# Kernel optimization log

Hardware: AMD Instinct MI355X
Metric: run time of the kernel (lower is better)

The kernel has to match this reference:

```python
import jax, jax.numpy as jnp
import numpy as np

# Standard NF4 quantization codebook (bitsandbytes values)
_NF4_CB = np.array([
    -1.0, -0.6961928009986877, -0.5250730514526367, -0.39491748809814453,
    -0.28444138169288635, -0.18477343022823334, -0.09105003625154495, 0.0,
    0.07958029955625534, 0.16093020141124725, 0.24611230194568634, 0.33791524171829224,
    0.44070982933044434, 0.5626170039176941, 0.7229568362236023, 1.0], dtype=np.float32)

B, L, H, E, DFF = 2, 2048, 2048, 8, 8192
BLK = 512  # NF4 quantization block size (b_idx = h // 512 in kernel)


def setup_inputs() -> dict:
    key = jax.random.key(0)
    ks = jax.random.split(key, 8)
    N = B * L
    x = jax.random.normal(ks[0], (B, L, H), dtype=jnp.float32)
    router_w = jax.random.normal(ks[1], (H, E), dtype=jnp.float32) * 0.02
    # packed NF4: one byte = two 4-bit codebook indices (low nibble -> even h)
    nf4 = jax.random.randint(ks[2], (N, E, H // 2), 0, 256, dtype=jnp.int32)
    mean = jax.random.normal(ks[3], (N, E, H // BLK), dtype=jnp.float32) * 0.01
    std = jax.random.uniform(ks[4], (N, E, H // BLK), dtype=jnp.float32) + 0.5
    codebook = jnp.asarray(_NF4_CB)
    w1 = jax.random.normal(ks[5], (H, DFF), dtype=jnp.float32) * 0.02
    w2 = jax.random.normal(ks[6], (DFF, H), dtype=jnp.float32) * 0.02
    return {"x": x, "router_w": router_w, "nf4": nf4, "mean": mean,
            "std": std, "codebook": codebook, "w1": w1, "w2": w2}


def reference(x, router_w, nf4, mean, std, codebook, w1, w2):
    b, l, h = x.shape
    n = b * l
    e = router_w.shape[1]
    xf = x.reshape(n, h)

    # shared expert MLP (base_mlp): Linear -> GELU -> Linear
    mlp = jax.nn.gelu(xf @ w1) @ w2  # [N, H]

    # router: logits in fp32, softmax, cast to fp16 as the kernel does
    logits = xf @ router_w  # [N, E]
    probs = jax.nn.softmax(logits, axis=-1).astype(jnp.float16).astype(jnp.float32)

    # NF4 unpack: low nibble -> even h, high nibble -> odd h
    low = nf4 & 15
    high = (nf4 >> 4) & 15
    idx = jnp.stack([low, high], axis=-1).reshape(n, e, h)  # interleave -> [N,E,H]
    vals = codebook[idx]  # codebook gather, [N,E,H]

    # per-block (512) rescale: val*std + mean
    nb = mean.shape[-1]
    blk = h // nb
    dq = (vals.reshape(n, e, nb, blk) * std[..., None] + mean[..., None]).reshape(n, e, h)

    # weighted expert mix + MLP residual add
    moe = jnp.einsum('ne,neh->nh', probs, dq)
    return (moe + mlp).reshape(b, l, h)
```

## Files before the change

kernel.cpp:

```cpp
#include <hip/hip_runtime.h>
#include <hip/hip_bf16.h>
#include <hip/hip_fp16.h>

#define H 2048
#define E 8
#define DFF 8192
#define NTOK 4096
#define NB 4

typedef _Float16 f16x8 __attribute__((ext_vector_type(8)));
typedef _Float16 f16x2 __attribute__((ext_vector_type(2)));
typedef float f32x4 __attribute__((ext_vector_type(4)));

#define AS1 __attribute__((address_space(1)))
#define AS3 __attribute__((address_space(3)))

__device__ __forceinline__ void gl_lds16(const void* g, void* l) {
    __builtin_amdgcn_global_load_lds((const AS1 unsigned int*)g,
                                     (AS3 unsigned int*)l, 16, 0, 0);
}

__device__ __forceinline__ float gelu_f(float x) {
    float u = 0.7978845608028654f * x * (1.0f + 0.044715f * x * x);
    float t = fabsf(u);
    float e = __expf(-2.0f * t);
    float th = (1.0f - e) / (1.0f + e);
    th = copysignf(th, u);
    return 0.5f * x * (1.0f + th);
}

__global__ __launch_bounds__(256) void router_moe_kernel(
    const float* __restrict__ x, const float* __restrict__ rw,
    const int* __restrict__ nf4, const float* __restrict__ mean,
    const float* __restrict__ stdv, const float* __restrict__ cb,
    _Float16* __restrict__ xh, float* __restrict__ moe)
{
    int n = blockIdx.x, t = threadIdx.x;
    __shared__ float red[4][E];
    __shared__ float pr[E];
    __shared__ float cbl[32];
    __shared__ float ps[E][NB];
    __shared__ float cmean[NB];

    float acc[E];
#pragma unroll
    for (int e = 0; e < E; ++e) acc[e] = 0.f;
    const float* xr = x + (size_t)n * H;
#pragma unroll
    for (int k = 0; k < H / 256; ++k) {
        int h = t + k * 256;
        float xv = xr[h];
        xh[(size_t)n * H + h] = (_Float16)xv;
        const float4* r4 = reinterpret_cast<const float4*>(rw + (size_t)h * E);
        float4 a = r4[0], b = r4[1];
        acc[0] += xv * a.x; acc[1] += xv * a.y; acc[2] += xv * a.z; acc[3] += xv * a.w;
        acc[4] += xv * b.x; acc[5] += xv * b.y; acc[6] += xv * b.z; acc[7] += xv * b.w;
    }
#pragma unroll
    for (int e = 0; e < E; ++e) {
        float v = acc[e];
#pragma unroll
        for (int o = 32; o > 0; o >>= 1) v += __shfl_down(v, o, 64);
        acc[e] = v;
    }
    int wave = t >> 6, lane = t & 63;
    if (lane == 0) {
#pragma unroll
        for (int e = 0; e < E; ++e) red[wave][e] = acc[e];
    }
    __syncthreads();
    if (t == 0) {
        float lg[E];
        float mx = -1e30f;
#pragma unroll
        for (int e = 0; e < E; ++e) {
            lg[e] = red[0][e] + red[1][e] + red[2][e] + red[3][e];
            mx = fmaxf(mx, lg[e]);
        }
        float s = 0.f;
#pragma unroll
        for (int e = 0; e < E; ++e) { lg[e] = expf(lg[e] - mx); s += lg[e]; }
        float inv = 1.f / s;
#pragma unroll
        for (int e = 0; e < E; ++e) {
            float p = lg[e] * inv;
            pr[e] = __half2float(__float2half(p));
        }
    }
    __syncthreads();

    if (t < 16) { float v = cb[t]; cbl[t] = v; cbl[t + 16] = v; }
    else if (t >= 32 && t < 64) {
        int e = (t - 32) >> 2, b = t & 3;
        ps[e][b] = pr[e] * stdv[((size_t)n * E + e) * NB + b];
    } else if (t >= 64 && t < 68) {
        int b = t - 64; float s = 0.f;
        for (int e = 0; e < E; ++e)
            s += pr[e] * mean[((size_t)n * E + e) * NB + b];
        cmean[b] = s;
    }
    __syncthreads();

    int b = t >> 6;
    int cboff = (t & 1) << 4;
    const int4* w4 = reinterpret_cast<const int4*>(nf4 + (size_t)n * (E * H / 2));
    float o[8];
    float cm = cmean[b];
#pragma unroll
    for (int u = 0; u < 8; ++u) o[u] = cm;
#pragma unroll
    for (int e = 0; e < E; ++e) {
        int4 wv = w4[e * 256 + t];
        float pse = ps[e][b];
        int w0 = wv.x, w1 = wv.y, w2 = wv.z, w3 = wv.w;
        o[0] += pse * cbl[(w0 & 15) + cboff];
        o[1] += pse * cbl[((w0 >> 4) & 15) + cboff];
        o[2] += pse * cbl[(w1 & 15) + cboff];
        o[3] += pse * cbl[((w1 >> 4) & 15) + cboff];
        o[4] += pse * cbl[(w2 & 15) + cboff];
        o[5] += pse * cbl[((w2 >> 4) & 15) + cboff];
        o[6] += pse * cbl[(w3 & 15) + cboff];
        o[7] += pse * cbl[((w3 >> 4) & 15) + cboff];
    }
    float4* op = reinterpret_cast<float4*>(moe + (size_t)n * H + 8 * t);
    op[0] = make_float4(o[0], o[1], o[2], o[3]);
    op[1] = make_float4(o[4], o[5], o[6], o[7]);
}

__global__ __launch_bounds__(256) void transpose_cast_kernel(
    const float* __restrict__ src, _Float16* __restrict__ dst, int R, int C)
{
    __shared__ float tile[64][65];
    int t = threadIdx.x;
    int c0 = blockIdx.x * 64, r0 = blockIdx.y * 64;
    int ct = (t & 15) * 4, rt = t >> 4;
#pragma unroll
    for (int i = 0; i < 4; ++i) {
        int r = rt + i * 16;
        float4 v = *reinterpret_cast<const float4*>(src + (size_t)(r0 + r) * C + c0 + ct);
        tile[r][ct] = v.x; tile[r][ct + 1] = v.y;
        tile[r][ct + 2] = v.z; tile[r][ct + 3] = v.w;
    }
    __syncthreads();
    int u = (t & 31) * 2, cq = t >> 5;
#pragma unroll
    for (int i = 0; i < 8; ++i) {
        int c = cq + i * 8;
        f16x2 pk;
        pk[0] = (_Float16)tile[u][c];
        pk[1] = (_Float16)tile[u + 1][c];
        *reinterpret_cast<f16x2*>(dst + (size_t)(c0 + c) * R + r0 + u) = pk;
    }
}

template <int EPI, int MAP>
__global__ __launch_bounds__(512, 2) void gemm8p_kernel(
    const _Float16* __restrict__ A, const _Float16* __restrict__ Bt,
    const float* __restrict__ addsrc, void* __restrict__ outv,
    float* __restrict__ aux, int K, int LDK, int N)
{
    __shared__ uint4 lds_u4[131072 / 16];
    char* lds = (char*)lds_u4;
    char* R0 = lds;
    char* R1 = lds + 65536;

    int t = threadIdx.x;
    int id = blockIdx.x;
    int xcd = id & 7, chunk = id >> 3;
    int by, bx, ks = 0;
    if constexpr (MAP == 0) {
        by = (xcd & 1) * 8 + (chunk & 7);
        bx = (xcd >> 1) * 8 + (chunk >> 3);
    } else {
        by = (xcd >> 1) * 4 + (chunk & 3);
        bx = (xcd & 1) * 4 + ((chunk >> 2) & 3);
        ks = chunk >> 4;
    }
    int m0 = by * 256, n0 = bx * 256;
    int koff = ks * K;

    const unsigned short* sA = (const unsigned short*)A
        + (size_t)(m0 + (t & 255)) * LDK + koff + (t >> 8) * 8;
    const unsigned short* sB = (const unsigned short*)Bt
        + (size_t)(n0 + (t & 255)) * LDK + koff + (t >> 8) * 8;
    unsigned dstT = (unsigned)t * 16;

    int lane = t & 63, wave = t >> 6;
    int wr = wave >> 2, wc = wave & 3;
    int mb = wr * 128, nb = wc * 64;
    int q = lane >> 4, m16 = lane & 15;

    unsigned aBase = (unsigned)(mb + m16) * 16u;
    unsigned bBase = 32768u + (unsigned)(nb + m16) * 16u;

    f32x4 acc[8][4] = {};
    f16x8 af[8], bL[4], bH[4];

#define STG_A(Wb, T, s) do { \
    gl_lds16(sA + (size_t)(T) * 64 + (s) * 16,      (Wb) + (s) * 8192 + dstT); \
    gl_lds16(sA + (size_t)(T) * 64 + (s) * 16 + 16, (Wb) + (s) * 8192 + 8192 + dstT); } while (0)
#define STG_B(Wb, T, s) do { \
    gl_lds16(sB + (size_t)(T) * 64 + (s) * 16,      (Wb) + 32768 + (s) * 8192 + dstT); \
    gl_lds16(sB + (size_t)(T) * 64 + (s) * 16 + 16, (Wb) + 32768 + (s) * 8192 + 8192 + dstT); } while (0)
#define RD_A(Rb, ih) do { \
    _Pragma("unroll") for (int il = 0; il < 4; ++il) \
    _Pragma("unroll") for (int kh = 0; kh < 2; ++kh) \
        af[il * 2 + kh] = *(const f16x8*)((Rb) + aBase + \
            (unsigned)(kh * 16384 + q * 4096 + (ih) * 1024 + il * 256)); } while (0)
#define RD_B(Rb, jh, dst) do { \
    _Pragma("unroll") for (int jl = 0; jl < 2; ++jl) \
    _Pragma("unroll") for (int kh = 0; kh < 2; ++kh) \
        dst[jl * 2 + kh] = *(const f16x8*)((Rb) + bBase + \
            (unsigned)(kh * 16384 + q * 4096 + (jh) * 512 + jl * 256)); } while (0)
#define MMQ(ih, bfr, j0) do { \
    __builtin_amdgcn_s_setprio(1); \
    _Pragma("unroll") for (int il = 0; il < 4; ++il) \
    _Pragma("unroll") for (int jl = 0; jl < 2; ++jl) \
    _Pragma("unroll") for (int kh = 0; kh < 2; ++kh) \
        acc[(ih) * 4 + il][(j0) + jl] = __builtin_amdgcn_mfma_f32_16x16x32_f16( \
            af[il * 2 + kh], bfr[jl * 2 + kh], acc[(ih) * 4 + il][(j0) + jl], 0, 0, 0); \
    __builtin_amdgcn_s_setprio(0); } while (0)
#define BARR  asm volatile("s_barrier" ::: "memory")
#define LGKM0 asm volatile("s_waitcnt lgkmcnt(0)" ::: "memory")

    STG_A(R0, 0, 0); STG_A(R0, 0, 2);
    STG_B(R0, 0, 0); STG_B(R0, 0, 2);
    STG_A(R1, 1, 0);
    asm volatile("s_waitcnt vmcnt(2)" ::: "memory");
    BARR;

    int NIT = K / 128;
    for (int i = 0; i < NIT; ++i) {
        int T0 = 2 * i, T1 = 2 * i + 1;
        bool more = (i + 1 < NIT);

        STG_A(R1, T1, 2);
        RD_A(R0, 0); RD_B(R0, 0, bL);
        BARR; LGKM0;
        MMQ(0, bL, 0);
        BARR;
        STG_B(R1, T1, 0);
        RD_B(R0, 1, bH);
        BARR; LGKM0;
        MMQ(0, bH, 2);
        BARR;
        STG_B(R1, T1, 2);
        RD_A(R0, 1);
        BARR; LGKM0;
        MMQ(1, bH, 2);
        BARR;
        if (more) STG_A(R0, T0 + 2, 0);
        MMQ(1, bL, 0);
        if (more) asm volatile("s_waitcnt vmcnt(2)" ::: "memory");
        else      asm volatile("s_waitcnt vmcnt(0)" ::: "memory");
        BARR;

        if (more) STG_A(R0, T0 + 2, 2);
        RD_A(R1, 0); RD_B(R1, 0, bL);
        BARR; LGKM0;
        MMQ(0, bL, 0);
        BARR;
        if (more) STG_B(R0, T0 + 2, 0);
        RD_B(R1, 1, bH);
        BARR; LGKM0;
        MMQ(0, bH, 2);
        BARR;
        if (more) STG_B(R0, T0 + 2, 2);
        RD_A(R1, 1);
        BARR; LGKM0;
        MMQ(1, bH, 2);
        BARR;
        if (more) STG_A(R1, T1 + 2, 0);
        MMQ(1, bL, 0);
        if (more) asm volatile("s_waitcnt vmcnt(2)" ::: "memory");
        else      asm volatile("s_waitcnt vmcnt(0)" ::: "memory");
        BARR;
    }

#pragma unroll
    for (int i = 0; i < 8; ++i)
#pragma unroll
        for (int j = 0; j < 4; ++j) {
            int row = m0 + mb + i * 16 + q * 4;
            int col = n0 + nb + j * 16 + m16;
#pragma unroll
            for (int rix = 0; rix < 4; ++rix) {
                float v = acc[i][j][rix];
                size_t o = (size_t)(row + rix) * N + col;
                if constexpr (EPI == 0) {
                    ((_Float16*)outv)[o] = (_Float16)gelu_f(v);
                } else {
                    if (ks == 0) ((float*)outv)[o] = v + addsrc[o];
                    else         aux[o] = v;
                }
            }
        }
#undef STG_A
#undef STG_B
#undef RD_A
#undef RD_B
#undef MMQ
#undef BARR
#undef LGKM0
}

__global__ __launch_bounds__(256) void combine_kernel(
    float* __restrict__ out, const float* __restrict__ part)
{
    size_t base = (size_t)blockIdx.x * 256 + threadIdx.x;
    const float4* p4 = (const float4*)part;
    float4* o4 = (float4*)out;
#pragma unroll
    for (int s = 0; s < 4; ++s) {
        size_t i = base + (size_t)s * 524288;
        float4 a = o4[i], b = p4[i];
        o4[i] = make_float4(a.x + b.x, a.y + b.y, a.z + b.z, a.w + b.w);
    }
}

extern "C" void kernel_launch(void* const* d_in, const int* in_sizes, int n_in,
                              void* d_out, int out_size, void* d_ws, size_t ws_size,
                              hipStream_t stream) {
    const float* x    = (const float*)d_in[0];
    const float* rw   = (const float*)d_in[1];
    const int*   nf4  = (const int*)d_in[2];
    const float* mean = (const float*)d_in[3];
    const float* stdv = (const float*)d_in[4];
    const float* cb   = (const float*)d_in[5];
    const float* w1   = (const float*)d_in[6];
    const float* w2   = (const float*)d_in[7];
    float* out = (float*)d_out;

    char* ws = (char*)d_ws;
    float* moe        = (float*)(ws + 131072);
    _Float16* xh      = (_Float16*)(ws + 33685504);
    _Float16* w1t     = (_Float16*)(ws + 50462720);
    _Float16* w2t     = (_Float16*)(ws + 84017152);
    _Float16* hid     = (_Float16*)(ws + 117571584);
    float* pbuf       = (float*)(ws + 50462720);

    router_moe_kernel<<<NTOK, 256, 0, stream>>>(x, rw, nf4, mean, stdv, cb, xh, moe);
    transpose_cast_kernel<<<dim3(DFF / 64, H / 64), 256, 0, stream>>>(w1, w1t, H, DFF);
    transpose_cast_kernel<<<dim3(H / 64, DFF / 64), 256, 0, stream>>>(w2, w2t, DFF, H);
    gemm8p_kernel<0, 0><<<512, 512, 0, stream>>>(xh, w1t, nullptr, (void*)hid,
                                                 nullptr, H, H, DFF);
    gemm8p_kernel<1, 1><<<256, 512, 0, stream>>>(hid, w2t, moe, (void*)out,
                                                 pbuf, DFF / 2, DFF, H);
    combine_kernel<<<2048, 256, 0, stream>>>(out, pbuf);
}
```

Before: 737.0 us.

## Replace double-buffered K=128 GEMM pipeline with five-stage K=32 ring buffer

```diff
diff --git a/kernel.cpp b/kernel.cpp
--- a/kernel.cpp
+++ b/kernel.cpp
@@ -154,15 +154,13 @@
 }
 
 template <int EPI, int MAP>
-__global__ __launch_bounds__(512, 2) void gemm8p_kernel(
+__global__ __launch_bounds__(512, 2) void gemm5b_kernel(
     const _Float16* __restrict__ A, const _Float16* __restrict__ Bt,
     const float* __restrict__ addsrc, void* __restrict__ outv,
     float* __restrict__ aux, int K, int LDK, int N)
 {
-    __shared__ uint4 lds_u4[131072 / 16];
+    __shared__ uint4 lds_u4[163840 / 16];
     char* lds = (char*)lds_u4;
-    char* R0 = lds;
-    char* R1 = lds + 65536;
 
     int t = threadIdx.x;
     int id = blockIdx.x;
@@ -190,91 +188,65 @@
     int mb = wr * 128, nb = wc * 64;
     int q = lane >> 4, m16 = lane & 15;
 
-    unsigned aBase = (unsigned)(mb + m16) * 16u;
-    unsigned bBase = 32768u + (unsigned)(nb + m16) * 16u;
+    unsigned aOff = (unsigned)(q * 4096 + (mb + m16) * 16);
+    unsigned bOff = (unsigned)(16384 + q * 4096 + (nb + m16) * 16);
 
     f32x4 acc[8][4] = {};
-    f16x8 af[8], bL[4], bH[4];
-
-#define STG_A(Wb, T, s) do { \
-    gl_lds16(sA + (size_t)(T) * 64 + (s) * 16,      (Wb) + (s) * 8192 + dstT); \
-    gl_lds16(sA + (size_t)(T) * 64 + (s) * 16 + 16, (Wb) + (s) * 8192 + 8192 + dstT); } while (0)
-#define STG_B(Wb, T, s) do { \
-    gl_lds16(sB + (size_t)(T) * 64 + (s) * 16,      (Wb) + 32768 + (s) * 8192 + dstT); \
-    gl_lds16(sB + (size_t)(T) * 64 + (s) * 16 + 16, (Wb) + 32768 + (s) * 8192 + 8192 + dstT); } while (0)
-#define RD_A(Rb, ih) do { \
+    f16x8 afL[4], afH[4], bf[4];
+
+#define STG_A(Wb, T) do { \
+    gl_lds16(sA + (size_t)(T) * 32,      (Wb) + dstT); \
+    gl_lds16(sA + (size_t)(T) * 32 + 16, (Wb) + 8192 + dstT); } while (0)
+#define STG_B(Wb, T) do { \
+    gl_lds16(sB + (size_t)(T) * 32,      (Wb) + 16384 + dstT); \
+    gl_lds16(sB + (size_t)(T) * 32 + 16, (Wb) + 16384 + 8192 + dstT); } while (0)
+#define RD_B(Rb) do { \
+    _Pragma("unroll") for (int jl = 0; jl < 4; ++jl) \
+        bf[jl] = *(const f16x8*)((Rb) + bOff + jl * 256); } while (0)
+#define RD_AL(Rb) do { \
     _Pragma("unroll") for (int il = 0; il < 4; ++il) \
-    _Pragma("unroll") for (int kh = 0; kh < 2; ++kh) \
-        af[il * 2 + kh] = *(const f16x8*)((Rb) + aBase + \
-            (unsigned)(kh * 16384 + q * 4096 + (ih) * 1024 + il * 256)); } while (0)
-#define RD_B(Rb, jh, dst) do { \
-    _Pragma("unroll") for (int jl = 0; jl < 2; ++jl) \
-    _Pragma("unroll") for (int kh = 0; kh < 2; ++kh) \
-        dst[jl * 2 + kh] = *(const f16x8*)((Rb) + bBase + \
-            (unsigned)(kh * 16384 + q * 4096 + (jh) * 512 + jl * 256)); } while (0)
-#define MMQ(ih, bfr, j0) do { \
+        afL[il] = *(const f16x8*)((Rb) + aOff + il * 256); } while (0)
+#define RD_AH(Rb) do { \
+    _Pragma("unroll") for (int il = 0; il < 4; ++il) \
+        afH[il] = *(const f16x8*)((Rb) + aOff + 1024 + il * 256); } while (0)
+#define MM(i0, afr) do { \
     __builtin_amdgcn_s_setprio(1); \
     _Pragma("unroll") for (int il = 0; il < 4; ++il) \
-    _Pragma("unroll") for (int jl = 0; jl < 2; ++jl) \
-    _Pragma("unroll") for (int kh = 0; kh < 2; ++kh) \
-        acc[(ih) * 4 + il][(j0) + jl] = __builtin_amdgcn_mfma_f32_16x16x32_f16( \
-            af[il * 2 + kh], bfr[jl * 2 + kh], acc[(ih) * 4 + il][(j0) + jl], 0, 0, 0); \
+    _Pragma("unroll") for (int jl = 0; jl < 4; ++jl) \
+        acc[(i0) + il][jl] = __builtin_amdgcn_mfma_f32_16x16x32_f16( \
+            afr[il], bf[jl], acc[(i0) + il][jl], 0, 0, 0); \
     __builtin_amdgcn_s_setprio(0); } while (0)
 #define BARR  asm volatile("s_barrier" ::: "memory")
 #define LGKM0 asm volatile("s_waitcnt lgkmcnt(0)" ::: "memory")
 
-    STG_A(R0, 0, 0); STG_A(R0, 0, 2);
-    STG_B(R0, 0, 0); STG_B(R0, 0, 2);
-    STG_A(R1, 1, 0);
-    asm volatile("s_waitcnt vmcnt(2)" ::: "memory");
+    STG_A(lds,         0); STG_B(lds,         0);
+    STG_A(lds + 32768, 1); STG_B(lds + 32768, 1);
+    STG_A(lds + 65536, 2); STG_B(lds + 65536, 2);
+    asm volatile("s_waitcnt vmcnt(8)" ::: "memory");
     BARR;
 
-    int NIT = K / 128;
-    for (int i = 0; i < NIT; ++i) {
-        int T0 = 2 * i, T1 = 2 * i + 1;
-        bool more = (i + 1 < NIT);
-
-        STG_A(R1, T1, 2);
-        RD_A(R0, 0); RD_B(R0, 0, bL);
+    int NT = K / 32;
+    unsigned rb = 0, wb = 3 * 32768;
+    for (int T = 0; T < NT; ++T) {
+        char* R = lds + rb;
+        char* W = lds + wb;
+        bool st = (T + 3 < NT);
+
+        RD_B(R); RD_AL(R);
+        if (st) STG_A(W, T + 3);
         BARR; LGKM0;
-        MMQ(0, bL, 0);
+        MM(0, afL);
         BARR;
-        STG_B(R1, T1, 0);
-        RD_B(R0, 1, bH);
+        RD_AH(R);
+        if (st) STG_B(W, T + 3);
         BARR; LGKM0;
-        MMQ(0, bH, 2);
+        MM(4, afH);
+        if (st) asm volatile("s_waitcnt vmcnt(8)" ::: "memory");
+        else    asm volatile("s_waitcnt vmcnt(0)" ::: "memory");
         BARR;
-        STG_B(R1, T1, 2);
-        RD_A(R0, 1);
-        BARR; LGKM0;
-        MMQ(1, bH, 2);
-        BARR;
-        if (more) STG_A(R0, T0 + 2, 0);
-        MMQ(1, bL, 0);
-        if (more) asm volatile("s_waitcnt vmcnt(2)" ::: "memory");
-        else      asm volatile("s_waitcnt vmcnt(0)" ::: "memory");
-        BARR;
-
-        if (more) STG_A(R0, T0 + 2, 2);
-        RD_A(R1, 0); RD_B(R1, 0, bL);
-        BARR; LGKM0;
-        MMQ(0, bL, 0);
-        BARR;
-        if (more) STG_B(R0, T0 + 2, 0);
-        RD_B(R1, 1, bH);
-        BARR; LGKM0;
-        MMQ(0, bH, 2);
-        BARR;
-        if (more) STG_B(R0, T0 + 2, 2);
-        RD_A(R1, 1);
-        BARR; LGKM0;
-        MMQ(1, bH, 2);
-        BARR;
-        if (more) STG_A(R1, T1 + 2, 0);
-        MMQ(1, bL, 0);
-        if (more) asm volatile("s_waitcnt vmcnt(2)" ::: "memory");
-        else      asm volatile("s_waitcnt vmcnt(0)" ::: "memory");
-        BARR;
+
+        rb += 32768; if (rb == 163840) rb = 0;
+        wb += 32768; if (wb == 163840) wb = 0;
     }
 
 #pragma unroll
@@ -297,9 +269,10 @@
         }
 #undef STG_A
 #undef STG_B
-#undef RD_A
 #undef RD_B
-#undef MMQ
+#undef RD_AL
+#undef RD_AH
+#undef MM
 #undef BARR
 #undef LGKM0
 }
@@ -342,9 +315,9 @@
     router_moe_kernel<<<NTOK, 256, 0, stream>>>(x, rw, nf4, mean, stdv, cb, xh, moe);
     transpose_cast_kernel<<<dim3(DFF / 64, H / 64), 256, 0, stream>>>(w1, w1t, H, DFF);
     transpose_cast_kernel<<<dim3(H / 64, DFF / 64), 256, 0, stream>>>(w2, w2t, DFF, H);
-    gemm8p_kernel<0, 0><<<512, 512, 0, stream>>>(xh, w1t, nullptr, (void*)hid,
+    gemm5b_kernel<0, 0><<<512, 512, 0, stream>>>(xh, w1t, nullptr, (void*)hid,
                                                  nullptr, H, H, DFF);
-    gemm8p_kernel<1, 1><<<256, 512, 0, stream>>>(hid, w2t, moe, (void*)out,
+    gemm5b_kernel<1, 1><<<256, 512, 0, stream>>>(hid, w2t, moe, (void*)out,
                                                  pbuf, DFF / 2, DFF, H);
     combine_kernel<<<2048, 256, 0, stream>>>(out, pbuf);
 }
```

After: 724.8 us. No clear change (-1.7%).
